# Optimization experiments

Measured on AMD Instinct MI355X. Metric: run time of the kernel, lower is better.

## Reference

```python
import jax, jax.numpy as jnp
import numpy as np

NUM_HEADS = 2
LN_EPS = 1e-5


def layer_norm(x, w, b):
    mu = jnp.mean(x, axis=-1, keepdims=True)
    var = jnp.mean(jnp.square(x - mu), axis=-1, keepdims=True)
    return (x - mu) * jax.lax.rsqrt(var + LN_EPS) * w + b


def setup_inputs() -> dict:
    key = jax.random.key(0)
    ks = jax.random.split(key, 8)
    B, N, C = 8, 2048, 1024
    H = 2 * C  # mlp hidden
    s = lambda fan_in: 1.0 / np.sqrt(fan_in)
    return {
        "x": jax.random.normal(ks[0], (B, N, C), dtype=jnp.float32),
        "ln1_w": jnp.ones((C,), jnp.float32),
        "ln1_b": jnp.zeros((C,), jnp.float32),
        "qkv_w": jax.random.normal(ks[1], (C, 3 * C), jnp.float32) * s(C),
        "qkv_b": jnp.zeros((3 * C,), jnp.float32),
        "proj_w": jax.random.normal(ks[2], (C, C), jnp.float32) * s(C),
        "proj_b": jnp.zeros((C,), jnp.float32),
        "ln2_w": jnp.ones((C,), jnp.float32),
        "ln2_b": jnp.zeros((C,), jnp.float32),
        "mlp_w1": jax.random.normal(ks[3], (C, H), jnp.float32) * s(C),
        "mlp_b1": jnp.zeros((H,), jnp.float32),
        "mlp_w2": jax.random.normal(ks[4], (H, C), jnp.float32) * s(H),
        "mlp_b2": jnp.zeros((C,), jnp.float32),
    }


def reference(x, ln1_w, ln1_b, qkv_w, qkv_b, proj_w, proj_b, ln2_w, ln2_b,
              mlp_w1, mlp_b1, mlp_w2, mlp_b2):
    B, N, C = x.shape
    h = NUM_HEADS
    d = C // h
    scale = d ** -0.5

    # --- attention branch ---
    xn = layer_norm(x, ln1_w, ln1_b)
    qkv = (xn @ qkv_w + qkv_b).reshape(B, N, 3, h, d)
    q, k, v = jnp.moveaxis(qkv, 2, 0)          # each [B, N, h, d]
    q = jnp.swapaxes(q, 1, 2)                  # [B, h, N, d]
    k = jnp.swapaxes(k, 1, 2)
    v = jnp.swapaxes(v, 1, 2)
    attn = jnp.einsum("bhnd,bhmd->bhnm", q, k) * scale
    attn = jax.nn.softmax(attn, axis=-1)       # [B, h, N, N]
    out = jnp.einsum("bhnm,bhmd->bhnd", attn, v)
    out = jnp.swapaxes(out, 1, 2).reshape(B, N, C)
    out = out @ proj_w + proj_b
    x = x + out

    # --- mlp branch ---
    xn = layer_norm(x, ln2_w, ln2_b)
    hdn = jax.nn.gelu(xn @ mlp_w1 + mlp_b1, approximate=False)
    x = x + (hdn @ mlp_w2 + mlp_b2)
    return x
```

## Files before the change

### kernel.cpp

```cpp
#include <hip/hip_runtime.h>
#include <hip/hip_bf16.h>
#include <math.h>

#define TILE 128
#define BK 32

using short8  = __attribute__((ext_vector_type(8))) short;
using short4v = __attribute__((ext_vector_type(4))) short;
using f32x4   = __attribute__((ext_vector_type(4))) float;
typedef __hip_bfloat16 bf16;

constexpr int BB = 8, SEQ = 2048, C = 1024, H3 = 3072, DH = 512, MH = 2048;
constexpr int MR = BB * SEQ;

enum {
  F_TRANSB = 1,
  F_GELU   = 2,
  F_RES    = 4,
  F_OUTBF16= 8,
  F_BIAS   = 16,
  F_SCALE  = 32,
  F_RESF32 = 64
};

struct ZOffs { long long a[16]; long long b[16]; long long c[16]; };

__device__ __forceinline__ float bf2f(bf16 h) { return __bfloat162float(h); }

__device__ __forceinline__ void gload16(const void* g, void* l) {
  __builtin_amdgcn_global_load_lds(
      (const __attribute__((address_space(1))) unsigned int*)g,
      (__attribute__((address_space(3))) unsigned int*)l, 16, 0, 0);
}

template<int FLAGS>
__global__ __launch_bounds__(256) void gemm_k(
    const bf16* __restrict__ A,
    const bf16* __restrict__ B,
    void* __restrict__ Dst,
    const float* __restrict__ bias,
    const void* __restrict__ res,
    int K, int lda, int ldb, int ldc,
    float scale, ZOffs zo)
{
  __shared__ __align__(16) unsigned short As[TILE * BK];
  __shared__ __align__(16) unsigned short Bs[TILE * BK];
  const int tid = threadIdx.x;
  const int z = blockIdx.z;
  const int m0 = blockIdx.y * TILE, n0 = blockIdx.x * TILE;
  const bf16* Ab = A + zo.a[z];
  const bf16* Bb = B + zo.b[z];
  const long long coff = zo.c[z];
  const int wave = tid >> 6, lane = tid & 63;
  const int wm = (wave & 1) << 6, wn = (wave >> 1) << 6;
  const int lr = lane & 15, lq = lane >> 4;

  int srow[2], skb[2];
  #pragma unroll
  for (int i = 0; i < 2; i++) {
    int c = tid + (i << 8);
    srow[i] = c >> 2;
    skb[i]  = (c & 3) ^ ((srow[i] >> 1) & 3);
  }
  const bf16* Asrc[2]; const bf16* Bsrc[2] = {nullptr, nullptr};
  #pragma unroll
  for (int i = 0; i < 2; i++)
    Asrc[i] = Ab + (size_t)(m0 + srow[i]) * lda + skb[i] * 8;
  if (FLAGS & F_TRANSB) {
    #pragma unroll
    for (int i = 0; i < 2; i++)
      Bsrc[i] = Bb + (size_t)(n0 + srow[i]) * ldb + skb[i] * 8;
  }

  f32x4 acc[4][4] = {};
  const int swl = (lr >> 1) & 3;

  for (int k0 = 0; k0 < K; k0 += BK) {
    #pragma unroll
    for (int i = 0; i < 2; i++)
      gload16(Asrc[i] + k0, &As[(tid + (i << 8)) * 8]);
    if (FLAGS & F_TRANSB) {
      #pragma unroll
      for (int i = 0; i < 2; i++)
        gload16(Bsrc[i] + k0, &Bs[(tid + (i << 8)) * 8]);
    } else {
      #pragma unroll
      for (int i = 0; i < 2; i++) {
        int c = tid + (i << 8);
        int kk = c >> 4, nn = (c & 15) << 3;
        unsigned short tmp[8];
        *(uint4*)tmp = *(const uint4*)(Bb + (size_t)(k0 + kk) * ldb + n0 + nn);
        #pragma unroll
        for (int j = 0; j < 8; j++) {
          int n = nn + j;
          Bs[n * BK + (((kk >> 3) ^ ((n >> 1) & 3)) << 3) + (kk & 7)] = tmp[j];
        }
      }
    }
    __syncthreads();
    short8 af[4], bfr[4];
    #pragma unroll
    for (int mi = 0; mi < 4; mi++)
      af[mi] = *(const short8*)&As[(wm + mi * 16 + lr) * BK + ((lq ^ swl) << 3)];
    #pragma unroll
    for (int ni = 0; ni < 4; ni++)
      bfr[ni] = *(const short8*)&Bs[(wn + ni * 16 + lr) * BK + ((lq ^ swl) << 3)];
    #pragma unroll
    for (int mi = 0; mi < 4; mi++)
      #pragma unroll
      for (int ni = 0; ni < 4; ni++)
        acc[mi][ni] = __builtin_amdgcn_mfma_f32_16x16x32_bf16(
            af[mi], bfr[ni], acc[mi][ni], 0, 0, 0);
    __syncthreads();
  }

  #pragma unroll
  for (int mi = 0; mi < 4; mi++) {
    #pragma unroll
    for (int ni = 0; ni < 4; ni++) {
      int col = n0 + wn + ni * 16 + lr;
      float bv = (FLAGS & F_BIAS) ? bias[col] : 0.0f;
      #pragma unroll
      for (int r = 0; r < 4; r++) {
        int row = m0 + wm + mi * 16 + lq * 4 + r;
        float v = acc[mi][ni][r];
        if (FLAGS & F_SCALE) v *= scale;
        v += bv;
        if (FLAGS & F_GELU) v = 0.5f * v * (1.0f + erff(v * 0.70710678118654752f));
        if (FLAGS & F_RES) {
          size_t ridx = (size_t)row * ldc + col;
          v += (FLAGS & F_RESF32) ? ((const float*)res)[ridx]
                                  : bf2f(((const bf16*)res)[ridx]);
        }
        size_t idx = (size_t)coff + (size_t)row * ldc + col;
        if (FLAGS & F_OUTBF16) ((bf16*)Dst)[idx] = __float2bfloat16(v);
        else                   ((float*)Dst)[idx] = v;
      }
    }
  }
}

template<int FLAGS>
__global__ __launch_bounds__(512, 2) void gemm256_k(
    const bf16* __restrict__ A,
    const bf16* __restrict__ B,
    void* __restrict__ Dst,
    const float* __restrict__ bias,
    const void* __restrict__ res,
    int K, int lda, int ldb, int ldc,
    float scale, ZOffs zo)
{
  static_assert(FLAGS & F_TRANSB, "gemm256_k requires B^T layout");
  extern __shared__ __align__(16) unsigned short smem[];

  const int tid = threadIdx.x;
  const int z = blockIdx.z;

  const int gx = gridDim.x;
  const int nwg = gx * gridDim.y;
  const int wg = blockIdx.y * gx + blockIdx.x;
  const int cpx = nwg >> 3;
  const int swz = (wg & 7) * cpx + (wg >> 3);
  const int m0 = (swz / gx) * 256, n0 = (swz % gx) * 256;

  const bf16* Ab = A + zo.a[z];
  const bf16* Bb = B + zo.b[z];
  const long long coff = zo.c[z];
  const int wave = tid >> 6, lane = tid & 63;
  const int wm = wave >> 2, wn = wave & 3;
  const int lr = lane & 15, lq = lane >> 4;
  const int r7 = lr & 7;
  const int sk0 = (lq ^ r7) << 3;
  const int sk1 = ((4 + lq) ^ r7) << 3;
  const int rowA = (wm * 128 + lr) * 64;
  const int rowB = (wn * 64 + lr) * 64;

  const int t8 = tid >> 3, s8 = tid & 7;
  const int sslot = (s8 ^ (t8 & 7)) << 3;
  const bf16* srcA = Ab + (size_t)(m0 + t8) * lda + sslot;
  const int rB0 = (t8 & 31) + ((t8 >> 5) << 6);
  const bf16* srcB = Bb + (size_t)(n0 + rB0) * ldb + sslot;
  const int dA0 = tid * 8;
  const int dB0 = rB0 * 64 + s8 * 8;

  const int nt = K >> 6;

#define SA(h_, ks_, Ad_)                                                       \
  do {                                                                         \
    gload16(srcA + (size_t)((h_) * 64) * lda + (ks_),                          \
            (Ad_) + dA0 + (h_) * 4096);                                        \
    gload16(srcA + (size_t)((h_) * 64 + 128) * lda + (ks_),                    \
            (Ad_) + dA0 + (h_) * 4096 + 8192);                                 \
  } while (0)
#define SB(h_, ks_, Bd_)                                                       \
  do {                                                                         \
    gload16(srcB + (size_t)((h_) * 32) * ldb + (ks_),                          \
            (Bd_) + dB0 + (h_) * 2048);                                        \
    gload16(srcB + (size_t)((h_) * 32 + 128) * ldb + (ks_),                    \
            (Bd_) + dB0 + (h_) * 2048 + 8192);                                 \
  } while (0)

  {
    const int npro = nt < 2 ? nt : 2;
    for (int t = 0; t < npro; ++t) {
      unsigned short* Ad = smem + (t & 1) * 16384;
      unsigned short* Bd = smem + 32768 + (t & 1) * 16384;
      const int ks = t * 64;
      SA(0, ks, Ad); SA(1, ks, Ad); SB(0, ks, Bd); SB(1, ks, Bd);
    }
  }

  f32x4 acc[8][4] = {};
  short8 af0[4], af1[4];
  short8 bA0[2], bA1[2];
  short8 bB0[2], bB1[2];

#define RD_AF(mh_)                                                             \
  _Pragma("unroll")                                                            \
  for (int m_ = 0; m_ < 4; ++m_) {                                             \
    af0[m_] = *(const short8*)&At[rowA + ((mh_) * 64 + m_ * 16) * 64 + sk0];   \
    af1[m_] = *(const short8*)&At[rowA + ((mh_) * 64 + m_ * 16) * 64 + sk1];   \
  }
#define RD_BF(nh_, b0_, b1_)                                                   \
  _Pragma("unroll")                                                            \
  for (int n_ = 0; n_ < 2; ++n_) {                                             \
    b0_[n_] = *(const short8*)&Bt[rowB + ((nh_) * 32 + n_ * 16) * 64 + sk0];   \
    b1_[n_] = *(const short8*)&Bt[rowB + ((nh_) * 32 + n_ * 16) * 64 + sk1];   \
  }
#define MM(mh_, nh_, b0_, b1_)                                                 \
  __builtin_amdgcn_s_setprio(1);                                               \
  _Pragma("unroll")                                                            \
  for (int m_ = 0; m_ < 4; ++m_)                                               \
    _Pragma("unroll")                                                          \
    for (int n_ = 0; n_ < 2; ++n_) {                                           \
      acc[(mh_) * 4 + m_][(nh_) * 2 + n_] =                                    \
          __builtin_amdgcn_mfma_f32_16x16x32_bf16(                             \
              af0[m_], b0_[n_], acc[(mh_) * 4 + m_][(nh_) * 2 + n_], 0, 0, 0); \
      acc[(mh_) * 4 + m_][(nh_) * 2 + n_] =                                    \
          __builtin_amdgcn_mfma_f32_16x16x32_bf16(                             \
              af1[m_], b1_[n_], acc[(mh_) * 4 + m_][(nh_) * 2 + n_], 0, 0, 0); \
    }                                                                          \
  __builtin_amdgcn_s_setprio(0);

  for (int t = 0; t < nt; ++t) {
    if (t == nt - 1) asm volatile("s_waitcnt vmcnt(0)" ::: "memory");
    else             asm volatile("s_waitcnt vmcnt(8)" ::: "memory");
    __builtin_amdgcn_s_barrier();

    const unsigned short* At = smem + (t & 1) * 16384;
    const unsigned short* Bt = smem + 32768 + (t & 1) * 16384;
    unsigned short* Ad = smem + (t & 1) * 16384;
    unsigned short* Bd = smem + 32768 + (t & 1) * 16384;
    const bool st = (t + 2) < nt;
    const int ks = (t + 2) * 64;

    RD_AF(0);
    RD_BF(0, bA0, bA1);
    __builtin_amdgcn_s_barrier();
    MM(0, 0, bA0, bA1);
    __builtin_amdgcn_s_barrier();

    RD_BF(1, bB0, bB1);
    if (st) { SA(0, ks, Ad); SB(0, ks, Bd); }
    __builtin_amdgcn_s_barrier();
    MM(0, 1, bB0, bB1);
    __builtin_amdgcn_s_barrier();

    RD_AF(1);
    if (st) { SB(1, ks, Bd); }
    __builtin_amdgcn_s_barrier();
    MM(1, 1, bB0, bB1);
    __builtin_amdgcn_s_barrier();

    if (st) { SA(1, ks, Ad); }
    MM(1, 0, bA0, bA1);
  }

#undef SA
#undef SB
#undef RD_AF
#undef RD_BF
#undef MM

  const int colBase = n0 + wn * 64 + lr;
  float bv[4];
  #pragma unroll
  for (int n = 0; n < 4; ++n)
    bv[n] = (FLAGS & F_BIAS) ? bias[colBase + n * 16] : 0.0f;
  #pragma unroll
  for (int m = 0; m < 8; ++m) {
    #pragma unroll
    for (int n = 0; n < 4; ++n) {
      const int col = colBase + n * 16;
      #pragma unroll
      for (int r = 0; r < 4; ++r) {
        const int row = m0 + wm * 128 + m * 16 + lq * 4 + r;
        float v = acc[m][n][r];
        if (FLAGS & F_SCALE) v *= scale;
        v += bv[n];
        if (FLAGS & F_GELU) v = 0.5f * v * (1.0f + erff(v * 0.70710678118654752f));
        if (FLAGS & F_RES) {
          size_t ridx = (size_t)row * ldc + col;
          v += (FLAGS & F_RESF32) ? ((const float*)res)[ridx]
                                  : bf2f(((const bf16*)res)[ridx]);
        }
        size_t idx = (size_t)coff + (size_t)row * ldc + col;
        if (FLAGS & F_OUTBF16) ((bf16*)Dst)[idx] = __float2bfloat16(v);
        else                   ((float*)Dst)[idx] = v;
      }
    }
  }
}

__global__ __launch_bounds__(256) void tconv_kernel(
    const float* __restrict__ src, bf16* __restrict__ dst, int K, int N)
{
  __shared__ float t[32][33];
  int n0 = blockIdx.x * 32, k0 = blockIdx.y * 32;
  int c = threadIdx.x & 31, r = threadIdx.x >> 5;
  #pragma unroll
  for (int i = 0; i < 4; i++)
    t[r + i * 8][c] = src[(size_t)(k0 + r + i * 8) * N + n0 + c];
  __syncthreads();
  #pragma unroll
  for (int i = 0; i < 4; i++)
    dst[(size_t)(n0 + r + i * 8) * K + k0 + c] = __float2bfloat16(t[c][r + i * 8]);
}

__global__ __launch_bounds__(256) void vtrans_kernel(
    const bf16* __restrict__ qkv, bf16* __restrict__ vt)
{
  __shared__ unsigned short t[32][33];
  int bh = blockIdx.z, b = bh >> 1, h = bh & 1;
  int n0 = blockIdx.x * 32, d0 = blockIdx.y * 32;
  int c = threadIdx.x & 31, r = threadIdx.x >> 5;
  const bf16* src = qkv + (size_t)b * SEQ * H3 + 2 * C + (size_t)h * DH;
  #pragma unroll
  for (int i = 0; i < 4; i++)
    t[r + i * 8][c] = *(const unsigned short*)&src[(size_t)(n0 + r + i * 8) * H3 + d0 + c];
  __syncthreads();
  bf16* dst = vt + ((size_t)bh * DH + d0) * SEQ + n0;
  #pragma unroll
  for (int i = 0; i < 4; i++)
    *(unsigned short*)&dst[(size_t)(r + i * 8) * SEQ + c] = t[c][r + i * 8];
}

__device__ __forceinline__ void ld4(const float* p, float v[4]) {
  const float4 t = *(const float4*)p;
  v[0] = t.x; v[1] = t.y; v[2] = t.z; v[3] = t.w;
}
__device__ __forceinline__ void ld4(const bf16* p, float v[4]) {
  short4v t = *(const short4v*)p;
  #pragma unroll
  for (int i = 0; i < 4; ++i) v[i] = bf2f(((const bf16*)&t)[i]);
}

template<typename T>
__global__ __launch_bounds__(256) void ln_kernel(
    const T* __restrict__ x,
    const float* __restrict__ w,
    const float* __restrict__ b,
    bf16* __restrict__ out)
{
  __shared__ float sm[4], sm2[4];
  int row = blockIdx.x, tid = threadIdx.x;
  float v[4];
  ld4(x + (size_t)row * 1024 + tid * 4, v);
  float s  = v[0] + v[1] + v[2] + v[3];
  float sq = v[0]*v[0] + v[1]*v[1] + v[2]*v[2] + v[3]*v[3];
  #pragma unroll
  for (int o = 32; o > 0; o >>= 1) {
    s  += __shfl_down(s, o, 64);
    sq += __shfl_down(sq, o, 64);
  }
  int wvi = tid >> 6, lnn = tid & 63;
  if (lnn == 0) { sm[wvi] = s; sm2[wvi] = sq; }
  __syncthreads();
  s  = sm[0] + sm[1] + sm[2] + sm[3];
  sq = sm2[0] + sm2[1] + sm2[2] + sm2[3];
  float mean = s * (1.0f / 1024.0f);
  float var  = sq * (1.0f / 1024.0f) - mean * mean;
  float rs = rsqrtf(var + 1e-5f);
  float wv4[4], bv4[4];
  ld4(w + tid * 4, wv4);
  ld4(b + tid * 4, bv4);
  short4v o4;
  #pragma unroll
  for (int i = 0; i < 4; ++i)
    ((bf16*)&o4)[i] = __float2bfloat16((v[i] - mean) * rs * wv4[i] + bv4[i]);
  *(short4v*)&out[(size_t)row * 1024 + tid * 4] = o4;
}

__global__ __launch_bounds__(256) void softmax_kernel(
    bf16* __restrict__ sc)
{
  __shared__ float sm[4];
  int tid = threadIdx.x;
  size_t base = ((size_t)blockIdx.y * 2048 + blockIdx.x) * 2048 + (size_t)tid * 8;
  short8 sv = *(const short8*)&sc[base];
  float v[8], m = -1e30f;
  #pragma unroll
  for (int i = 0; i < 8; i++) { v[i] = bf2f(((const bf16*)&sv)[i]); m = fmaxf(m, v[i]); }
  #pragma unroll
  for (int o = 32; o > 0; o >>= 1) m = fmaxf(m, __shfl_down(m, o, 64));
  int wvi = tid >> 6, lnn = tid & 63;
  if (lnn == 0) sm[wvi] = m;
  __syncthreads();
  m = fmaxf(fmaxf(sm[0], sm[1]), fmaxf(sm[2], sm[3]));
  __syncthreads();
  float s = 0.f;
  #pragma unroll
  for (int i = 0; i < 8; i++) { v[i] = __expf(v[i] - m); s += v[i]; }
  #pragma unroll
  for (int o = 32; o > 0; o >>= 1) s += __shfl_down(s, o, 64);
  if (lnn == 0) sm[wvi] = s;
  __syncthreads();
  s = sm[0] + sm[1] + sm[2] + sm[3];
  float inv = 1.0f / s;
  short8 ov;
  #pragma unroll
  for (int i = 0; i < 8; i++)
    ((bf16*)&ov)[i] = __float2bfloat16(v[i] * inv);
  *(short8*)&sc[base] = ov;
}

#define G256(FL, grid_, A_, B_, D_, bias_, res_, K_, lda_, ldb_, ldc_, sc_, zo_)      \
  do {                                                                                \
    (void)hipFuncSetAttribute(reinterpret_cast<const void*>(&gemm256_k<(FL)>),        \
                              hipFuncAttributeMaxDynamicSharedMemorySize, 131072);    \
    hipLaunchKernelGGL((gemm256_k<(FL)>), grid_, dim3(512), 131072, stream,           \
                       A_, B_, D_, bias_, res_, K_, lda_, ldb_, ldc_, sc_, zo_);      \
  } while (0)

extern "C" void kernel_launch(void* const* d_in, const int* in_sizes, int n_in,
                              void* d_out, int out_size, void* d_ws, size_t ws_size,
                              hipStream_t stream) {
  const float* x      = (const float*)d_in[0];
  const float* ln1_w  = (const float*)d_in[1];
  const float* ln1_b  = (const float*)d_in[2];
  const float* qkv_w  = (const float*)d_in[3];
  const float* qkv_b  = (const float*)d_in[4];
  const float* proj_w = (const float*)d_in[5];
  const float* proj_b = (const float*)d_in[6];
  const float* ln2_w  = (const float*)d_in[7];
  const float* ln2_b  = (const float*)d_in[8];
  const float* mlp_w1 = (const float*)d_in[9];
  const float* mlp_b1 = (const float*)d_in[10];
  const float* mlp_w2 = (const float*)d_in[11];
  const float* mlp_b2 = (const float*)d_in[12];
  float* out = (float*)d_out;

  char* ws = (char*)d_ws;
  const size_t MB = 1ull << 20;
  bf16* qkvT  = (bf16*)ws;
  bf16* projT = qkvT + 3 * 1024 * 1024;
  bf16* w1T   = qkvT + 4 * 1024 * 1024;
  bf16* w2T   = qkvT + 6 * 1024 * 1024;
  bf16* xn    = (bf16*)(ws + 16 * MB);
  bf16* qkvb  = (bf16*)(ws + 48 * MB);
  bf16* h1    = qkvb;
  bf16* Vt    = (bf16*)(ws + 144 * MB);

  int CH; bool useVt, x1f32;
  if      (ws_size >= 304 * MB) { CH = 16; useVt = true;  x1f32 = true;  }
  else if (ws_size >= 240 * MB) { CH = 8;  useVt = true;  x1f32 = true;  }
  else if (ws_size >= 208 * MB) { CH = 4;  useVt = true;  x1f32 = false; }
  else                          { CH = 4;  useVt = false; x1f32 = false; }
  char* R = ws + (useVt ? 176 * MB : 144 * MB);
  bf16*  scores = (bf16*)R;
  float* x1f    = (float*)R;
  bf16*  x1h    = (bf16*)R;

  ZOffs z0 = {};
  const float scale = 0.04419417382415922f;
  dim3 blk(256);

  hipLaunchKernelGGL(tconv_kernel, dim3(H3 / 32, C / 32), blk, 0, stream, qkv_w, qkvT, C, H3);
  hipLaunchKernelGGL(tconv_kernel, dim3(C / 32, C / 32), blk, 0, stream, proj_w, projT, C, C);
  hipLaunchKernelGGL(tconv_kernel, dim3(MH / 32, C / 32), blk, 0, stream, mlp_w1, w1T, C, MH);
  hipLaunchKernelGGL(tconv_kernel, dim3(C / 32, MH / 32), blk, 0, stream, mlp_w2, w2T, MH, C);

  hipLaunchKernelGGL((ln_kernel<float>), dim3(MR), blk, 0, stream, x, ln1_w, ln1_b, xn);

  G256(F_TRANSB | F_BIAS | F_OUTBF16, dim3(H3 / 256, MR / 256, 1),
       xn, qkvT, (void*)qkvb, qkv_b, nullptr, C, C, C, H3, 1.0f, z0);

  if (useVt)
    hipLaunchKernelGGL(vtrans_kernel, dim3(SEQ / 32, DH / 32, 16), blk, 0, stream, qkvb, Vt);

  for (int ch = 0; ch < 16 / CH; ch++) {
    ZOffs zq = {}, zp = {};
    for (int zz = 0; zz < CH; zz++) {
      int bh = ch * CH + zz, b = bh >> 1, hh = bh & 1;
      zq.a[zz] = (long long)b * SEQ * H3 + (long long)hh * DH;
      zq.b[zz] = (long long)b * SEQ * H3 + C + (long long)hh * DH;
      zq.c[zz] = (long long)zz * SEQ * SEQ;
      zp.a[zz] = (long long)zz * SEQ * SEQ;
      zp.b[zz] = useVt ? (long long)bh * DH * SEQ
                       : (long long)b * SEQ * H3 + 2 * C + (long long)hh * DH;
      zp.c[zz] = (long long)b * SEQ * C + (long long)hh * DH;
    }
    G256(F_TRANSB | F_SCALE | F_OUTBF16, dim3(SEQ / 256, SEQ / 256, CH),
         qkvb, qkvb, (void*)scores, nullptr, nullptr, DH, H3, H3, SEQ, scale, zq);
    hipLaunchKernelGGL(softmax_kernel, dim3(SEQ, CH), blk, 0, stream, scores);
    if (useVt)
      G256(F_TRANSB | F_OUTBF16, dim3(DH / 256, SEQ / 256, CH),
           scores, Vt, (void*)xn, nullptr, nullptr, SEQ, SEQ, SEQ, C, 1.0f, zp);
    else
      hipLaunchKernelGGL((gemm_k<F_OUTBF16>),
                         dim3(DH / TILE, SEQ / TILE, CH), blk, 0, stream,
                         scores, qkvb, (void*)xn, nullptr, nullptr, SEQ, SEQ, H3, C, 1.0f, zp);
  }

  if (x1f32) {
    G256(F_TRANSB | F_BIAS | F_RES | F_RESF32, dim3(C / 256, MR / 256, 1),
         xn, projT, (void*)x1f, proj_b, (const void*)x, C, C, C, C, 1.0f, z0);
    hipLaunchKernelGGL((ln_kernel<float>), dim3(MR), blk, 0, stream, x1f, ln2_w, ln2_b, xn);
  } else {
    G256(F_TRANSB | F_BIAS | F_RES | F_RESF32 | F_OUTBF16, dim3(C / 256, MR / 256, 1),
         xn, projT, (void*)x1h, proj_b, (const void*)x, C, C, C, C, 1.0f, z0);
    hipLaunchKernelGGL((ln_kernel<bf16>), dim3(MR), blk, 0, stream, x1h, ln2_w, ln2_b, xn);
  }

  G256(F_TRANSB | F_BIAS | F_GELU | F_OUTBF16, dim3(MH / 256, MR / 256, 1),
       xn, w1T, (void*)h1, mlp_b1, nullptr, C, C, C, MH, 1.0f, z0);

  if (x1f32) {
    G256(F_TRANSB | F_BIAS | F_RES | F_RESF32, dim3(C / 256, MR / 256, 1),
         h1, w2T, (void*)out, mlp_b2, (const void*)x1f, MH, MH, MH, C, 1.0f, z0);
  } else {
    G256(F_TRANSB | F_BIAS | F_RES, dim3(C / 256, MR / 256, 1),
         h1, w2T, (void*)out, mlp_b2, (const void*)x1h, MH, MH, MH, C, 1.0f, z0);
  }
}
```

Before: 765.5 us.

## Restructure GEMM main loop into k-half phases with deferred A-tile prefetch

Reorganizes the GEMM inner loop so each phase works on one k-half, reading all four B fragments for that half, instead of splitting by N-halves. Global-to-LDS stores for the next tiles are rescheduled: the second A half for tile t+1 is issued one iteration later, and the wait counts are adjusted to match. The goal is better overlap of LDS reads, global loads and MFMA work, with lower register pressure from fewer live fragments. The cost is more LDS fragment reads per iteration, since A fragments are re-read for each k-half, plus a more delicate vmcnt accounting that could race if it is wrong.

```diff
diff --git a/kernel.cpp b/kernel.cpp
--- a/kernel.cpp
+++ b/kernel.cpp
@@ -211,76 +211,73 @@
   }
 
   f32x4 acc[8][4] = {};
-  short8 af0[4], af1[4];
-  short8 bA0[2], bA1[2];
-  short8 bB0[2], bB1[2];
-
-#define RD_AF(mh_)                                                             \
+  short8 af[4], bk0[4], bk1[4];
+
+#define RD_AF(mh_, sk_)                                                        \
   _Pragma("unroll")                                                            \
-  for (int m_ = 0; m_ < 4; ++m_) {                                             \
-    af0[m_] = *(const short8*)&At[rowA + ((mh_) * 64 + m_ * 16) * 64 + sk0];   \
-    af1[m_] = *(const short8*)&At[rowA + ((mh_) * 64 + m_ * 16) * 64 + sk1];   \
-  }
-#define RD_BF(nh_, b0_, b1_)                                                   \
+  for (int m_ = 0; m_ < 4; ++m_)                                               \
+    af[m_] = *(const short8*)&At[rowA + ((mh_) * 64 + m_ * 16) * 64 + (sk_)];
+#define RD_BF(b_, sk_)                                                         \
   _Pragma("unroll")                                                            \
-  for (int n_ = 0; n_ < 2; ++n_) {                                             \
-    b0_[n_] = *(const short8*)&Bt[rowB + ((nh_) * 32 + n_ * 16) * 64 + sk0];   \
-    b1_[n_] = *(const short8*)&Bt[rowB + ((nh_) * 32 + n_ * 16) * 64 + sk1];   \
-  }
-#define MM(mh_, nh_, b0_, b1_)                                                 \
+  for (int n_ = 0; n_ < 4; ++n_)                                               \
+    b_[n_] = *(const short8*)&Bt[rowB + (n_ * 16) * 64 + (sk_)];
+#define MM16(mh_, b_)                                                          \
   __builtin_amdgcn_s_setprio(1);                                               \
   _Pragma("unroll")                                                            \
   for (int m_ = 0; m_ < 4; ++m_)                                               \
     _Pragma("unroll")                                                          \
-    for (int n_ = 0; n_ < 2; ++n_) {                                           \
-      acc[(mh_) * 4 + m_][(nh_) * 2 + n_] =                                    \
+    for (int n_ = 0; n_ < 4; ++n_)                                             \
+      acc[(mh_) * 4 + m_][n_] =                                                \
           __builtin_amdgcn_mfma_f32_16x16x32_bf16(                             \
-              af0[m_], b0_[n_], acc[(mh_) * 4 + m_][(nh_) * 2 + n_], 0, 0, 0); \
-      acc[(mh_) * 4 + m_][(nh_) * 2 + n_] =                                    \
-          __builtin_amdgcn_mfma_f32_16x16x32_bf16(                             \
-              af1[m_], b1_[n_], acc[(mh_) * 4 + m_][(nh_) * 2 + n_], 0, 0, 0); \
-    }                                                                          \
+              af[m_], b_[n_], acc[(mh_) * 4 + m_][n_], 0, 0, 0);               \
   __builtin_amdgcn_s_setprio(0);
 
   for (int t = 0; t < nt; ++t) {
-    if (t == nt - 1) asm volatile("s_waitcnt vmcnt(0)" ::: "memory");
-    else             asm volatile("s_waitcnt vmcnt(8)" ::: "memory");
+    if (t == 0)           asm volatile("s_waitcnt vmcnt(8)" ::: "memory");
+    else if (t == nt - 1) asm volatile("s_waitcnt vmcnt(0)" ::: "memory");
+    else                  asm volatile("s_waitcnt vmcnt(6)" ::: "memory");
     __builtin_amdgcn_s_barrier();
 
     const unsigned short* At = smem + (t & 1) * 16384;
     const unsigned short* Bt = smem + 32768 + (t & 1) * 16384;
-    unsigned short* Ad = smem + (t & 1) * 16384;
-    unsigned short* Bd = smem + 32768 + (t & 1) * 16384;
-    const bool st = (t + 2) < nt;
-    const int ks = (t + 2) * 64;
-
-    RD_AF(0);
-    RD_BF(0, bA0, bA1);
-    __builtin_amdgcn_s_barrier();
-    MM(0, 0, bA0, bA1);
-    __builtin_amdgcn_s_barrier();
-
-    RD_BF(1, bB0, bB1);
-    if (st) { SA(0, ks, Ad); SB(0, ks, Bd); }
-    __builtin_amdgcn_s_barrier();
-    MM(0, 1, bB0, bB1);
-    __builtin_amdgcn_s_barrier();
-
-    RD_AF(1);
-    if (st) { SB(1, ks, Bd); }
-    __builtin_amdgcn_s_barrier();
-    MM(1, 1, bB0, bB1);
-    __builtin_amdgcn_s_barrier();
-
-    if (st) { SA(1, ks, Ad); }
-    MM(1, 0, bA0, bA1);
+
+    RD_AF(0, sk0);
+    RD_BF(bk0, sk0);
+    if (t > 0 && t + 1 < nt) {
+      unsigned short* Ad = smem + ((t + 1) & 1) * 16384;
+      SA(1, (t + 1) * 64, Ad);
+    }
+    __builtin_amdgcn_s_barrier();
+    MM16(0, bk0);
+    __builtin_amdgcn_s_barrier();
+
+    RD_AF(0, sk1);
+    RD_BF(bk1, sk1);
+    __builtin_amdgcn_s_barrier();
+    MM16(0, bk1);
+    __builtin_amdgcn_s_barrier();
+
+    RD_AF(1, sk1);
+    if (t + 2 < nt) {
+      unsigned short* Ad = smem + (t & 1) * 16384;
+      unsigned short* Bd = smem + 32768 + (t & 1) * 16384;
+      const int ks = (t + 2) * 64;
+      SA(0, ks, Ad); SB(0, ks, Bd); SB(1, ks, Bd);
+    }
+    __builtin_amdgcn_s_barrier();
+    MM16(1, bk1);
+    __builtin_amdgcn_s_barrier();
+
+    RD_AF(1, sk0);
+    __builtin_amdgcn_s_barrier();
+    MM16(1, bk0);
   }
 
 #undef SA
 #undef SB
 #undef RD_AF
 #undef RD_BF
-#undef MM
+#undef MM16
 
   const int colBase = n0 + wn * 64 + lr;
   float bv[4];
```

Measured after the change: 789.0 us. 3.1% more time.
